# Optimization experiments

Hardware: AMD Instinct MI355X
Metric: run time of the kernel (lower is better)

The kernel has to match this reference:

```python
import jax, jax.numpy as jnp
import numpy as np

N_NODES = 100000   # m for both sparse matmuls (graph adjacency is N x N)
ITERATIONS = 10
ALPHA = 0.1
N_FEATURES = 2000
HIDDEN = 64
N_LABELS = 16
NNZ_FEAT = 5000000
N_EDGES = 3200000


def setup_inputs() -> dict:
    key = jax.random.key(0)
    ks = jax.random.split(key, 10)
    feat_rows = jax.random.randint(ks[0], (NNZ_FEAT,), 0, N_NODES, dtype=jnp.int32)
    feat_cols = jax.random.randint(ks[1], (NNZ_FEAT,), 0, N_FEATURES, dtype=jnp.int32)
    feature_values = jax.random.uniform(ks[2], (NNZ_FEAT,), dtype=jnp.float32)
    edge_rows = jax.random.randint(ks[3], (N_EDGES,), 0, N_NODES, dtype=jnp.int32)
    edge_cols = jax.random.randint(ks[4], (N_EDGES,), 0, N_NODES, dtype=jnp.int32)
    edge_weights = jax.random.uniform(ks[5], (N_EDGES,), dtype=jnp.float32) * (1.0 / 32.0)
    W1 = jax.random.normal(ks[6], (N_FEATURES, HIDDEN), dtype=jnp.float32) * 0.05
    b1 = jax.random.normal(ks[7], (HIDDEN,), dtype=jnp.float32) * 0.05
    W2 = jax.random.normal(ks[8], (HIDDEN, N_LABELS), dtype=jnp.float32) * 0.1
    b2 = jax.random.normal(ks[9], (N_LABELS,), dtype=jnp.float32) * 0.1
    return {"feat_rows": feat_rows, "feat_cols": feat_cols, "feature_values": feature_values,
            "edge_rows": edge_rows, "edge_cols": edge_cols, "edge_weights": edge_weights,
            "W1": W1, "b1": b1, "W2": W2, "b2": b2}


def spmm(rows, cols, vals, matrix, m):
    # sparse [m, k] (COO) @ dense [k, d]: gather rows of dense, scale, scatter-add
    out = matrix[cols] * vals[:, None]          # [nnz, d]
    return jax.ops.segment_sum(out, rows, num_segments=m)


def reference(feat_rows, feat_cols, feature_values, edge_rows, edge_cols,
              edge_weights, W1, b1, W2, b2):
    # layer 1: sparse features [N, F] @ W1 [F, H] + b1  (eval mode: dropout is identity)
    latent1 = spmm(feat_rows, feat_cols, feature_values, W1, N_NODES) + b1  # [N, H]
    latent1 = jax.nn.relu(latent1)
    z = latent1 @ W2 + b2                       # [N, L] local predictions

    def step(p, _):
        new = spmm(edge_rows, edge_cols, edge_weights, p, N_NODES)  # A_hat @ p
        p = (1.0 - ALPHA) * new + ALPHA * z
        return p, None

    preds, _ = jax.lax.scan(step, z, None, length=ITERATIONS)
    return jax.nn.log_softmax(preds, axis=1)
```

## Files before the change

kernel.cpp:

```cpp
#include <hip/hip_runtime.h>

#define N_NODES    100000
#define N_FEATURES 2000
#define HIDDEN     64
#define N_LABELS   16
#define NNZ_FEAT   5000000
#define N_EDGES    3200000
#define ITERS      10
#define ALPHA      0.1f

#define CBSH       9
#define CROWS      (1 << CBSH)
#define NBC        ((N_NODES + CROWS - 1) >> CBSH)
#define TILE       8192
#define NFB        ((NNZ_FEAT + TILE - 1) / TILE)
#define NEB        ((N_EDGES + TILE - 1) / TILE)
#define BCAP       28672

#define EQMUL  1048544.0f
#define EWDEC  (0.028125f / 32767.0f)

__device__ __forceinline__ unsigned short f2bf(float x) {
    unsigned u = __float_as_uint(x);
    u += 0x7FFF + ((u >> 16) & 1);
    return (unsigned short)(u >> 16);
}
__device__ __forceinline__ float bf_lo(unsigned u) { return __uint_as_float(u << 16); }
__device__ __forceinline__ float bf_hi(unsigned u) { return __uint_as_float(u & 0xFFFF0000u); }

__device__ __forceinline__ unsigned char f2fp8(float x) {
    float a = fabsf(x) * 16.0f;
    a = fminf(fmaxf(a, 0.015625f), 448.0f);
    unsigned u = __float_as_uint(a) + 0x80000;
    int v11 = (int)((u >> 20) & 0x7FF) - 960;
    v11 = v11 < 8 ? 8 : (v11 > 126 ? 126 : v11);
    return (unsigned char)(v11 | ((__float_as_uint(x) >> 24) & 0x80));
}
#if __has_builtin(__builtin_amdgcn_cvt_f32_fp8)
#define FP8DEC(w, s) __builtin_amdgcn_cvt_f32_fp8((w), (s))
#else
__device__ __forceinline__ float fp8dec_sw(unsigned w, int s) {
    unsigned u = (w >> (8 * s)) & 0xFF;
    return __uint_as_float((((u & 0x7F) + 960) << 20) | ((u & 0x80) << 24));
}
#define FP8DEC(w, s) fp8dec_sw((w), (s))
#endif


__global__ __launch_bounds__(256) void zero_int(int* __restrict__ p, int n) {
    int t = blockIdx.x * 256 + threadIdx.x;
    if (t < n) p[t] = 0;
}

__global__ __launch_bounds__(256) void hist2_k(const int* __restrict__ frows, int nf,
                                               int* __restrict__ cbf,
                                               const int* __restrict__ erows, int ne,
                                               int* __restrict__ cbe) {
    __shared__ int h[4 * NBC];
    for (int i = threadIdx.x; i < 4 * NBC; i += 256) h[i] = 0;
    __syncthreads();
    const int* rows; int n; int* dst; int b0, nb;
    if (blockIdx.x < 1280) { rows = frows; n = nf; dst = cbf; b0 = blockIdx.x; nb = 1280; }
    else                   { rows = erows; n = ne; dst = cbe; b0 = blockIdx.x - 1280; nb = 768; }
    int off = (threadIdx.x & 3) * NBC;
    int stride = nb * 256;
    for (int i = b0 * 256 + threadIdx.x; i < n; i += stride)
        atomicAdd(&h[off + (rows[i] >> CBSH)], 1);
    __syncthreads();
    for (int i = threadIdx.x; i < NBC; i += 256) {
        int v = h[i] + h[NBC + i] + h[2 * NBC + i] + h[3 * NBC + i];
        if (v) atomicAdd(&dst[i], v);
    }
}

__global__ __launch_bounds__(256) void scan2_k(const int* __restrict__ cbf,
                                               int* __restrict__ cbasef, int* __restrict__ gbf,
                                               int* __restrict__ frp,
                                               const int* __restrict__ cbe,
                                               int* __restrict__ cbasee, int* __restrict__ gbe,
                                               int* __restrict__ erp) {
    const int* cnt; int* cbase; int* gbcur; int* rp;
    if (blockIdx.x == 0) { cnt = cbf; cbase = cbasef; gbcur = gbf; rp = frp; }
    else                 { cnt = cbe; cbase = cbasee; gbcur = gbe; rp = erp; }
    __shared__ int s[256];
    int t = threadIdx.x;
    int v = (t < NBC) ? cnt[t] : 0;
    s[t] = v;
    __syncthreads();
    for (int off = 1; off < 256; off <<= 1) {
        int a = (t >= off) ? s[t - off] : 0;
        __syncthreads();
        s[t] += a;
        __syncthreads();
    }
    if (t < NBC) { cbase[t] = s[t] - v; gbcur[t] = s[t] - v; }
    if (t == NBC - 1) { cbase[NBC] = s[t]; rp[N_NODES] = s[t]; }
}

__global__ __launch_bounds__(1024) void binA2_k(
    const int* __restrict__ frows, const int* __restrict__ fcols, const float* __restrict__ fvals,
    int* __restrict__ gbf, int* __restrict__ fpk, unsigned short* __restrict__ frl,
    const int* __restrict__ erows, const int* __restrict__ ecols, const float* __restrict__ evals,
    int* __restrict__ gbe, int* __restrict__ epk, unsigned short* __restrict__ erl)
{
    __shared__ int            staged_pk[TILE];
    __shared__ unsigned short staged_rl[TILE];
    __shared__ unsigned char  sbkt[TILE];
    __shared__ int cnt0[NBC];
    __shared__ int cnt1[NBC];
    __shared__ int rstart[NBC];
    __shared__ int gbase[NBC];
    __shared__ int sc[256];

    const int* rows; const int* cols; const float* vals;
    int* gbcur; int* bpk; unsigned short* brl;
    int n, qshift, bfval; float qmul;
    int bid = blockIdx.x;
    if (bid < NFB) {
        rows = frows; cols = fcols; vals = fvals; gbcur = gbf; bpk = fpk; brl = frl;
        n = NNZ_FEAT; qshift = 16; qmul = 0.f; bfval = 1;
    } else {
        bid -= NFB;
        rows = erows; cols = ecols; vals = evals; gbcur = gbe; bpk = epk; brl = erl;
        n = N_EDGES; qshift = 17; qmul = EQMUL; bfval = 0;
    }

    int tid = threadIdx.x;
    int base = bid * TILE;
    int m = n - base; if (m > TILE) m = TILE;

    for (int i = tid; i < NBC; i += 1024) { cnt0[i] = 0; cnt1[i] = 0; }
    __syncthreads();

    int c = tid & 1;
    int* cntc = c ? cnt1 : cnt0;
    int seq[TILE / 1024];
    int rbuf[TILE / 1024];
    #pragma unroll
    for (int k = 0; k < TILE / 1024; ++k) {
        int j = k * 1024 + tid;
        if (j < m) {
            int r = rows[base + j];
            rbuf[k] = r;
            seq[k] = atomicAdd(&cntc[r >> CBSH], 1);
        }
    }
    __syncthreads();

    if (tid < 256) sc[tid] = (tid < NBC) ? (cnt0[tid] + cnt1[tid]) : 0;
    __syncthreads();
    for (int off = 1; off < 256; off <<= 1) {
        int a = 0;
        if (tid < 256 && tid >= off) a = sc[tid - off];
        __syncthreads();
        if (tid < 256) sc[tid] += a;
        __syncthreads();
    }
    if (tid < NBC) rstart[tid] = sc[tid] - (cnt0[tid] + cnt1[tid]);
    __syncthreads();

    #pragma unroll
    for (int k = 0; k < TILE / 1024; ++k) {
        int j = k * 1024 + tid;
        if (j < m) {
            int r = rbuf[k];
            int b = r >> CBSH;
            float v = vals[base + j];
            int q = bfval ? (int)f2bf(v) : __float2int_rn(v * qmul);
            int slot = rstart[b] + (c ? cnt0[b] : 0) + seq[k];
            staged_pk[slot] = (q << qshift) | cols[base + j];
            staged_rl[slot] = (unsigned short)(r & (CROWS - 1));
            sbkt[slot] = (unsigned char)b;
        }
    }
    __syncthreads();

    if (tid < NBC) {
        int tot = cnt0[tid] + cnt1[tid];
        if (tot > 0) gbase[tid] = atomicAdd(&gbcur[tid], tot);
    }
    __syncthreads();

    #pragma unroll
    for (int k = 0; k < TILE / 1024; ++k) {
        int slot = k * 1024 + tid;
        if (slot < m) {
            int b = sbkt[slot];
            int dst = gbase[b] + (slot - rstart[b]);
            bpk[dst] = staged_pk[slot];
            brl[dst] = staged_rl[slot];
        }
    }
}

__global__ __launch_bounds__(1024) void binB3_k(
    const int* __restrict__ fpk, const unsigned short* __restrict__ frl,
    const int* __restrict__ cbasef, int* __restrict__ frp, int* __restrict__ fcw,
    const int* __restrict__ epk, const unsigned short* __restrict__ erl,
    const int* __restrict__ cbasee, int* __restrict__ erp, int* __restrict__ ecw)
{
    const int* bin_pk; const unsigned short* bin_rl; const int* cbase; int* rp; int* cw;
    int b = blockIdx.x;
    if (b < NBC) { bin_pk = fpk; bin_rl = frl; cbase = cbasef; rp = frp; cw = fcw; }
    else { b -= NBC; bin_pk = epk; bin_rl = erl; cbase = cbasee; rp = erp; cw = ecw; }

    int r0 = b << CBSH;
    int nrows = N_NODES - r0; if (nrows > CROWS) nrows = CROWS;
    __shared__ int staged[BCAP];
    __shared__ int hist[CROWS];
    __shared__ int sc[CROWS];
    int t = threadIdx.x;
    if (t < CROWS) hist[t] = 0;
    __syncthreads();
    int s = cbase[b], e = cbase[b + 1];
    int cnt = e - s;
    for (int i = s + t; i < e; i += 1024)
        atomicAdd(&hist[bin_rl[i]], 1);
    __syncthreads();
    if (t < CROWS) sc[t] = hist[t];
    __syncthreads();
    for (int off = 1; off < CROWS; off <<= 1) {
        int a = (t >= off && t < CROWS) ? sc[t - off] : 0;
        __syncthreads();
        if (t < CROWS) sc[t] += a;
        __syncthreads();
    }
    if (t < CROWS) {
        int excl = sc[t] - hist[t];
        if (t < nrows) rp[r0 + t] = excl + s;
        hist[t] = excl;
    }
    __syncthreads();

    if (cnt <= BCAP) {
        for (int i = s + t; i < e; i += 1024) {
            int pos = atomicAdd(&hist[bin_rl[i]], 1);
            staged[pos] = bin_pk[i];
        }
        __syncthreads();
        for (int j = t; j < cnt; j += 1024)
            cw[s + j] = staged[j];
    } else {
        for (int i = s + t; i < e; i += 1024) {
            int pos = atomicAdd(&hist[bin_rl[i]], 1);
            cw[s + pos] = bin_pk[i];
        }
    }
}


__global__ __launch_bounds__(256) void w1_to_fp8(const float* __restrict__ W1,
                                                 unsigned char* __restrict__ W1q) {
    int t = blockIdx.x * 256 + threadIdx.x;
    if (t < N_FEATURES * HIDDEN / 4) {
        float4 v = reinterpret_cast<const float4*>(W1)[t];
        uchar4 o;
        o.x = f2fp8(v.x); o.y = f2fp8(v.y); o.z = f2fp8(v.z); o.w = f2fp8(v.w);
        reinterpret_cast<uchar4*>(W1q)[t] = o;
    }
}

__global__ __launch_bounds__(256) void spmm_fused(const int* __restrict__ rp,
                                                  const int* __restrict__ cwp,
                                                  const unsigned char* __restrict__ W1q,
                                                  const float* __restrict__ b1,
                                                  const float* __restrict__ W2,
                                                  const float* __restrict__ b2,
                                                  unsigned short* __restrict__ az,
                                                  unsigned short* __restrict__ pb0) {
    __shared__ float sW2T[N_LABELS * (HIDDEN + 1)];
    __shared__ float sb1[HIDDEN];
    __shared__ float sb2[N_LABELS];
    for (int i = threadIdx.x; i < HIDDEN * N_LABELS; i += 256) {
        int h = i >> 4, l = i & 15;
        sW2T[l * (HIDDEN + 1) + h] = W2[i];
    }
    if (threadIdx.x < HIDDEN) sb1[threadIdx.x] = b1[threadIdx.x];
    if (threadIdx.x < N_LABELS) sb2[threadIdx.x] = b2[threadIdx.x];
    __syncthreads();

    int t = blockIdx.x * 256 + threadIdx.x;
    int row = t >> 3, sl = t & 7;
    if (row >= N_NODES) return;
    int s = rp[row], e = rp[row + 1];
    int hbase = sl * 8;

    float acc[8];
    #pragma unroll
    for (int j = 0; j < 8; ++j) acc[j] = 0.f;

    int i = s;
    for (; i + 3 < e; i += 4) {
        uint2 wv[4]; float vv[4];
        #pragma unroll
        for (int k = 0; k < 4; ++k) {
            int pk = cwp[i + k];
            vv[k] = bf_hi((unsigned)pk);
            wv[k] = *reinterpret_cast<const uint2*>(W1q + (size_t)(pk & 0x7FF) * HIDDEN + hbase);
        }
        #pragma unroll
        for (int k = 0; k < 4; ++k) {
            acc[0] = fmaf(vv[k], FP8DEC(wv[k].x, 0), acc[0]);
            acc[1] = fmaf(vv[k], FP8DEC(wv[k].x, 1), acc[1]);
            acc[2] = fmaf(vv[k], FP8DEC(wv[k].x, 2), acc[2]);
            acc[3] = fmaf(vv[k], FP8DEC(wv[k].x, 3), acc[3]);
            acc[4] = fmaf(vv[k], FP8DEC(wv[k].y, 0), acc[4]);
            acc[5] = fmaf(vv[k], FP8DEC(wv[k].y, 1), acc[5]);
            acc[6] = fmaf(vv[k], FP8DEC(wv[k].y, 2), acc[6]);
            acc[7] = fmaf(vv[k], FP8DEC(wv[k].y, 3), acc[7]);
        }
    }
    for (; i < e; ++i) {
        int pk = cwp[i];
        float v = bf_hi((unsigned)pk);
        uint2 w = *reinterpret_cast<const uint2*>(W1q + (size_t)(pk & 0x7FF) * HIDDEN + hbase);
        acc[0] = fmaf(v, FP8DEC(w.x, 0), acc[0]);
        acc[1] = fmaf(v, FP8DEC(w.x, 1), acc[1]);
        acc[2] = fmaf(v, FP8DEC(w.x, 2), acc[2]);
        acc[3] = fmaf(v, FP8DEC(w.x, 3), acc[3]);
        acc[4] = fmaf(v, FP8DEC(w.y, 0), acc[4]);
        acc[5] = fmaf(v, FP8DEC(w.y, 1), acc[5]);
        acc[6] = fmaf(v, FP8DEC(w.y, 2), acc[6]);
        acc[7] = fmaf(v, FP8DEC(w.y, 3), acc[7]);
    }

    float part[16];
    #pragma unroll
    for (int l = 0; l < 16; ++l) part[l] = 0.f;
    #pragma unroll
    for (int j = 0; j < 8; ++j) {
        float a = fmaf(acc[j], 0.0625f, sb1[hbase + j]);
        a = a > 0.f ? a : 0.f;
        #pragma unroll
        for (int l = 0; l < 16; ++l)
            part[l] = fmaf(a, sW2T[l * (HIDDEN + 1) + hbase + j], part[l]);
    }
    #pragma unroll
    for (int l = 0; l < 8; ++l) {
        float lo = __shfl_xor(part[l], 1);
        float hi = __shfl_xor(part[l + 8], 1);
        part[l] = (sl & 1) ? (part[l + 8] + hi) : (part[l] + lo);
    }
    #pragma unroll
    for (int l = 0; l < 4; ++l) {
        float lo = __shfl_xor(part[l], 2);
        float hi = __shfl_xor(part[l + 4], 2);
        part[l] = (sl & 2) ? (part[l + 4] + hi) : (part[l] + lo);
    }
    #pragma unroll
    for (int l = 0; l < 2; ++l) {
        float lo = __shfl_xor(part[l], 4);
        float hi = __shfl_xor(part[l + 2], 4);
        part[l] = (sl & 4) ? (part[l + 2] + hi) : (part[l] + lo);
    }
    int lbase = 8 * (sl & 1) + 4 * ((sl >> 1) & 1) + 2 * ((sl >> 2) & 1);
    float z0 = part[0] + sb2[lbase];
    float z1 = part[1] + sb2[lbase + 1];
    unsigned oz = (unsigned)f2bf(z0) | ((unsigned)f2bf(z1) << 16);
    unsigned oa = (unsigned)f2bf(ALPHA * z0) | ((unsigned)f2bf(ALPHA * z1) << 16);
    *reinterpret_cast<unsigned*>(pb0 + (size_t)row * N_LABELS + lbase) = oz;
    *reinterpret_cast<unsigned*>(az  + (size_t)row * N_LABELS + lbase) = oa;
}

__global__ __launch_bounds__(256) void prop_bf16(const int* __restrict__ rp,
                                                 const int* __restrict__ cwp,
                                                 const unsigned short* __restrict__ az,
                                                 const unsigned short* __restrict__ pin,
                                                 unsigned short* __restrict__ pout) {
    int t = blockIdx.x * 256 + threadIdx.x;
    int row = t >> 3, sub = t & 7;
    if (row >= N_NODES) return;
    int s = rp[row], e = rp[row + 1];
    unsigned azw = *reinterpret_cast<const unsigned*>(az + (size_t)row * N_LABELS + sub * 2);
    float a0 = bf_lo(azw), a1 = bf_hi(azw);
    int i = s;
    for (; i + 7 < e; i += 8) {
        int cwv = cwp[i + sub];
        unsigned q[8]; float w[8];
        #pragma unroll
        for (int k = 0; k < 8; ++k) {
            int pk = __shfl(cwv, k, 8);
            w[k] = (float)((unsigned)pk >> 17) * EWDEC;
            q[k] = *reinterpret_cast<const unsigned*>(pin + (size_t)(pk & 0x1FFFF) * N_LABELS + sub * 2);
        }
        #pragma unroll
        for (int k = 0; k < 8; ++k) {
            a0 = fmaf(w[k], bf_lo(q[k]), a0);
            a1 = fmaf(w[k], bf_hi(q[k]), a1);
        }
    }
    for (; i < e; ++i) {
        int pk = cwp[i];
        float w = (float)((unsigned)pk >> 17) * EWDEC;
        unsigned q = *reinterpret_cast<const unsigned*>(pin + (size_t)(pk & 0x1FFFF) * N_LABELS + sub * 2);
        a0 = fmaf(w, bf_lo(q), a0);
        a1 = fmaf(w, bf_hi(q), a1);
    }
    *reinterpret_cast<unsigned*>(pout + (size_t)row * N_LABELS + sub * 2) =
        (unsigned)f2bf(a0) | ((unsigned)f2bf(a1) << 16);
}

__global__ __launch_bounds__(256) void prop_final(const int* __restrict__ rp,
                                                  const int* __restrict__ cwp,
                                                  const unsigned short* __restrict__ az,
                                                  const unsigned short* __restrict__ pin,
                                                  float* __restrict__ out) {
    int t = blockIdx.x * 256 + threadIdx.x;
    int row = t >> 3, sub = t & 7;
    if (row >= N_NODES) return;
    int s = rp[row], e = rp[row + 1];
    unsigned azw = *reinterpret_cast<const unsigned*>(az + (size_t)row * N_LABELS + sub * 2);
    float a0 = bf_lo(azw), a1 = bf_hi(azw);
    int i = s;
    for (; i + 7 < e; i += 8) {
        int cwv = cwp[i + sub];
        unsigned q[8]; float w[8];
        #pragma unroll
        for (int k = 0; k < 8; ++k) {
            int pk = __shfl(cwv, k, 8);
            w[k] = (float)((unsigned)pk >> 17) * EWDEC;
            q[k] = *reinterpret_cast<const unsigned*>(pin + (size_t)(pk & 0x1FFFF) * N_LABELS + sub * 2);
        }
        #pragma unroll
        for (int k = 0; k < 8; ++k) {
            a0 = fmaf(w[k], bf_lo(q[k]), a0);
            a1 = fmaf(w[k], bf_hi(q[k]), a1);
        }
    }
    for (; i < e; ++i) {
        int pk = cwp[i];
        float w = (float)((unsigned)pk >> 17) * EWDEC;
        unsigned q = *reinterpret_cast<const unsigned*>(pin + (size_t)(pk & 0x1FFFF) * N_LABELS + sub * 2);
        a0 = fmaf(w, bf_lo(q), a0);
        a1 = fmaf(w, bf_hi(q), a1);
    }
    float m = fmaxf(a0, a1);
    m = fmaxf(m, __shfl_xor(m, 1));
    m = fmaxf(m, __shfl_xor(m, 2));
    m = fmaxf(m, __shfl_xor(m, 4));
    float ssum = __expf(a0 - m) + __expf(a1 - m);
    ssum += __shfl_xor(ssum, 1);
    ssum += __shfl_xor(ssum, 2);
    ssum += __shfl_xor(ssum, 4);
    float lse = m + __logf(ssum);
    *reinterpret_cast<float2*>(out + (size_t)row * N_LABELS + sub * 2) =
        make_float2(a0 - lse, a1 - lse);
}


__global__ __launch_bounds__(256) void zero_f4(float4* __restrict__ p, int n4) {
    int t = blockIdx.x * 256 + threadIdx.x;
    if (t < n4) p[t] = make_float4(0.f, 0.f, 0.f, 0.f);
}

__global__ __launch_bounds__(256) void spmm_feat_atomic(
    const int* __restrict__ rows, const int* __restrict__ cols,
    const float* __restrict__ vals, const float* __restrict__ W1,
    float* __restrict__ latent)
{
    long long t = (long long)blockIdx.x * 256 + threadIdx.x;
    if (t >= (long long)NNZ_FEAT * 16) return;
    int e  = (int)(t >> 4);
    int dg = (int)(t & 15);
    int r = rows[e]; int c = cols[e]; float v = vals[e];
    float4 w = *reinterpret_cast<const float4*>(W1 + (size_t)c * HIDDEN + dg * 4);
    float* dst = latent + (size_t)r * HIDDEN + dg * 4;
    atomicAdd(dst + 0, v * w.x); atomicAdd(dst + 1, v * w.y);
    atomicAdd(dst + 2, v * w.z); atomicAdd(dst + 3, v * w.w);
}

__global__ __launch_bounds__(256) void compute_z(const float* __restrict__ latent,
                                                 const float* __restrict__ b1,
                                                 const float* __restrict__ W2,
                                                 const float* __restrict__ b2,
                                                 float* __restrict__ z) {
    __shared__ float sW2[HIDDEN * N_LABELS];
    __shared__ float sb1[HIDDEN];
    for (int i = threadIdx.x; i < HIDDEN * N_LABELS; i += 256) sW2[i] = W2[i];
    if (threadIdx.x < HIDDEN) sb1[threadIdx.x] = b1[threadIdx.x];
    __syncthreads();
    int t = blockIdx.x * 256 + threadIdx.x;
    int node = t >> 4;
    int l = t & 15;
    if (node >= N_NODES) return;
    float acc = b2[l];
    const float* lat = latent + (size_t)node * HIDDEN;
    #pragma unroll 8
    for (int h = 0; h < HIDDEN; ++h) {
        float a = lat[h] + sb1[h];
        a = a > 0.f ? a : 0.f;
        acc = fmaf(a, sW2[h * N_LABELS + l], acc);
    }
    z[(size_t)node * N_LABELS + l] = acc;
}

__global__ __launch_bounds__(256) void init_acc(const float* __restrict__ z,
                                                float* __restrict__ acc) {
    int t = blockIdx.x * 256 + threadIdx.x;
    if (t < N_NODES * N_LABELS / 4) {
        float4 zv = reinterpret_cast<const float4*>(z)[t];
        reinterpret_cast<float4*>(acc)[t] =
            make_float4(ALPHA * zv.x, ALPHA * zv.y, ALPHA * zv.z, ALPHA * zv.w);
    }
}

__global__ __launch_bounds__(256) void edge_scatter(
    const int* __restrict__ rows, const int* __restrict__ cols,
    const float* __restrict__ w, const float* __restrict__ p,
    float* __restrict__ acc)
{
    long long t = (long long)blockIdx.x * 256 + threadIdx.x;
    if (t >= (long long)N_EDGES * 4) return;
    int e = (int)(t >> 2);
    int part = (int)(t & 3);
    int r = rows[e]; int c = cols[e];
    float wt = w[e] * (1.0f - ALPHA);
    float4 pv = *reinterpret_cast<const float4*>(p + (size_t)c * N_LABELS + part * 4);
    float* dst = acc + (size_t)r * N_LABELS + part * 4;
    atomicAdd(dst + 0, wt * pv.x); atomicAdd(dst + 1, wt * pv.y);
    atomicAdd(dst + 2, wt * pv.z); atomicAdd(dst + 3, wt * pv.w);
}

__global__ __launch_bounds__(256) void logsoftmax_k(const float* __restrict__ p,
                                                    float* __restrict__ out) {
    int node = blockIdx.x * 256 + threadIdx.x;
    if (node >= N_NODES) return;
    const float4* src = reinterpret_cast<const float4*>(p + (size_t)node * N_LABELS);
    float4 a = src[0], b = src[1], c = src[2], d = src[3];
    float x[16] = {a.x,a.y,a.z,a.w, b.x,b.y,b.z,b.w, c.x,c.y,c.z,c.w, d.x,d.y,d.z,d.w};
    float m = x[0];
    #pragma unroll
    for (int i = 1; i < 16; ++i) m = fmaxf(m, x[i]);
    float s = 0.f;
    #pragma unroll
    for (int i = 0; i < 16; ++i) s += expf(x[i] - m);
    float lse = m + logf(s);
    float4* o = reinterpret_cast<float4*>(out + (size_t)node * N_LABELS);
    o[0] = make_float4(x[0]-lse,  x[1]-lse,  x[2]-lse,  x[3]-lse);
    o[1] = make_float4(x[4]-lse,  x[5]-lse,  x[6]-lse,  x[7]-lse);
    o[2] = make_float4(x[8]-lse,  x[9]-lse,  x[10]-lse, x[11]-lse);
    o[3] = make_float4(x[12]-lse, x[13]-lse, x[14]-lse, x[15]-lse);
}


extern "C" void kernel_launch(void* const* d_in, const int* in_sizes, int n_in,
                              void* d_out, int out_size, void* d_ws, size_t ws_size,
                              hipStream_t stream)
{
    const int*   feat_rows = (const int*)d_in[0];
    const int*   feat_cols = (const int*)d_in[1];
    const float* feat_vals = (const float*)d_in[2];
    const int*   edge_rows = (const int*)d_in[3];
    const int*   edge_cols = (const int*)d_in[4];
    const float* edge_w    = (const float*)d_in[5];
    const float* W1 = (const float*)d_in[6];
    const float* b1 = (const float*)d_in[7];
    const float* W2 = (const float*)d_in[8];
    const float* b2 = (const float*)d_in[9];
    float* out = (float*)d_out;

    size_t need = 0;
    size_t o_feat_cw = need; need += (size_t)NNZ_FEAT;
    size_t o_edge_cw = need; need += (size_t)N_EDGES;
    size_t o_latent  = need; need += (size_t)N_NODES * HIDDEN;
    size_t o_z       = need; need += (size_t)N_NODES * N_LABELS;
    size_t o_p0      = need; need += (size_t)N_NODES * N_LABELS;
    size_t o_p1      = need; need += (size_t)N_NODES * N_LABELS;
    size_t o_frp     = need; need += N_NODES + 1;
    size_t o_erp     = need; need += N_NODES + 1;
    size_t o_w1q     = need; need += (size_t)N_FEATURES * HIDDEN / 4;
    size_t o_ebin_pk = need; need += (size_t)N_EDGES;
    size_t o_ebin_rl = need; need += (size_t)N_EDGES / 2;
    size_t o_cbf     = need; need += NBC;
    size_t o_cbe     = need; need += NBC;
    size_t o_cbasef  = need; need += NBC + 1;
    size_t o_cbasee  = need; need += NBC + 1;
    size_t o_gbf     = need; need += NBC;
    size_t o_gbe     = need; need += NBC;
    size_t need_bytes = need * 4 + 64;

    float* base = (float*)d_ws;
    float* latent = base + o_latent;
    float* z  = base + o_z;
    float* p0 = base + o_p0;
    float* p1 = base + o_p1;

    if (ws_size >= need_bytes) {
        int* feat_cw = (int*)(base + o_feat_cw);
        int* edge_cw = (int*)(base + o_edge_cw);
        int* feat_rp = (int*)(base + o_frp);
        int* edge_rp = (int*)(base + o_erp);
        unsigned char* W1q = (unsigned char*)(base + o_w1q);
        int* cbf    = (int*)(base + o_cbf);
        int* cbe    = (int*)(base + o_cbe);
        int* cbasef = (int*)(base + o_cbasef);
        int* cbasee = (int*)(base + o_cbasee);
        int* gbf    = (int*)(base + o_gbf);
        int* gbe    = (int*)(base + o_gbe);
        int*            fbin_pk = (int*)(base + o_latent);
        unsigned short* fbin_rl = (unsigned short*)(base + o_z);
        int*            ebin_pk = (int*)(base + o_ebin_pk);
        unsigned short* ebin_rl = (unsigned short*)(base + o_ebin_rl);
        unsigned short* az  = (unsigned short*)z;
        unsigned short* pb0 = (unsigned short*)p0;
        unsigned short* pb1 = (unsigned short*)p1;

        w1_to_fp8<<<(N_FEATURES * HIDDEN / 4 + 255) / 256, 256, 0, stream>>>(W1, W1q);
        zero_int<<<2, 256, 0, stream>>>(cbf, 2 * NBC);
        hist2_k<<<2048, 256, 0, stream>>>(feat_rows, NNZ_FEAT, cbf, edge_rows, N_EDGES, cbe);
        scan2_k<<<2, 256, 0, stream>>>(cbf, cbasef, gbf, feat_rp, cbe, cbasee, gbe, edge_rp);
        binA2_k<<<NFB + NEB, 1024, 0, stream>>>(
            feat_rows, feat_cols, feat_vals, gbf, fbin_pk, fbin_rl,
            edge_rows, edge_cols, edge_w, gbe, ebin_pk, ebin_rl);
        binB3_k<<<2 * NBC, 1024, 0, stream>>>(
            fbin_pk, fbin_rl, cbasef, feat_rp, feat_cw,
            ebin_pk, ebin_rl, cbasee, edge_rp, edge_cw);

        spmm_fused<<<(N_NODES * 8 + 255) / 256, 256, 0, stream>>>(
            feat_rp, feat_cw, W1q, b1, W2, b2, az, pb0);

        const unsigned short* pin = pb0;
        int pgrid = (N_NODES * 8 + 255) / 256;
        for (int it = 0; it < ITERS - 1; ++it) {
            unsigned short* pout = (it & 1) ? pb0 : pb1;
            prop_bf16<<<pgrid, 256, 0, stream>>>(edge_rp, edge_cw, az, pin, pout);
            pin = pout;
        }
        prop_final<<<pgrid, 256, 0, stream>>>(edge_rp, edge_cw, az, pin, out);
    } else {
        int n4 = N_NODES * HIDDEN / 4;
        zero_f4<<<(n4 + 255) / 256, 256, 0, stream>>>((float4*)latent, n4);
        long long total = (long long)NNZ_FEAT * 16;
        spmm_feat_atomic<<<(int)((total + 255) / 256), 256, 0, stream>>>(
            feat_rows, feat_cols, feat_vals, W1, latent);
        compute_z<<<N_NODES * 16 / 256, 256, 0, stream>>>(latent, b1, W2, b2, z);
        const float* pin = z;
        float* bufs[2] = {p0, p1};
        for (int it = 0; it < ITERS; ++it) {
            float* pout = bufs[it & 1];
            init_acc<<<(N_NODES * N_LABELS / 4 + 255) / 256, 256, 0, stream>>>(z, pout);
            long long tot = (long long)N_EDGES * 4;
            edge_scatter<<<(int)((tot + 255) / 256), 256, 0, stream>>>(
                edge_rows, edge_cols, edge_w, pin, pout);
            pin = pout;
        }
        logsoftmax_k<<<(N_NODES + 255) / 256, 256, 0, stream>>>(pin, out);
    }
}
```

Before: 461.4 us.

## Vectorize COO loads in histogram/binning and stage fp8 W1 in shared memory

The histogram kernel now reads row indices as int4 and does four shared atomics per load. The binning kernel gives each thread 8 contiguous entries read with vector loads, and it drops the two-way split counters in favour of a single counter array. The fused feature SpMM stages the whole fp8 W1 (padded stride 9) into LDS and runs 1024-thread blocks, so the W1 gather hits shared memory instead of global. Risks: roughly 144KB of LDS per block limits occupancy to one block per CU and adds a staging cost per block, and the int4 histogram loop silently drops any tail when n is not a multiple of 4.

```diff
diff --git a/kernel.cpp b/kernel.cpp
--- a/kernel.cpp
+++ b/kernel.cpp
@@ -64,8 +64,15 @@
     else                   { rows = erows; n = ne; dst = cbe; b0 = blockIdx.x - 1280; nb = 768; }
     int off = (threadIdx.x & 3) * NBC;
     int stride = nb * 256;
-    for (int i = b0 * 256 + threadIdx.x; i < n; i += stride)
-        atomicAdd(&h[off + (rows[i] >> CBSH)], 1);
+    int n4 = n >> 2;
+    const int4* rows4 = reinterpret_cast<const int4*>(rows);
+    for (int i = b0 * 256 + threadIdx.x; i < n4; i += stride) {
+        int4 r = rows4[i];
+        atomicAdd(&h[off + (r.x >> CBSH)], 1);
+        atomicAdd(&h[off + (r.y >> CBSH)], 1);
+        atomicAdd(&h[off + (r.z >> CBSH)], 1);
+        atomicAdd(&h[off + (r.w >> CBSH)], 1);
+    }
     __syncthreads();
     for (int i = threadIdx.x; i < NBC; i += 256) {
         int v = h[i] + h[NBC + i] + h[2 * NBC + i] + h[3 * NBC + i];
@@ -106,8 +113,7 @@
     __shared__ int            staged_pk[TILE];
     __shared__ unsigned short staged_rl[TILE];
     __shared__ unsigned char  sbkt[TILE];
-    __shared__ int cnt0[NBC];
-    __shared__ int cnt1[NBC];
+    __shared__ int cnt[NBC];
     __shared__ int rstart[NBC];
     __shared__ int gbase[NBC];
     __shared__ int sc[256];
@@ -129,25 +135,39 @@
     int base = bid * TILE;
     int m = n - base; if (m > TILE) m = TILE;
 
-    for (int i = tid; i < NBC; i += 1024) { cnt0[i] = 0; cnt1[i] = 0; }
-    __syncthreads();
-
-    int c = tid & 1;
-    int* cntc = c ? cnt1 : cnt0;
-    int seq[TILE / 1024];
-    int rbuf[TILE / 1024];
-    #pragma unroll
-    for (int k = 0; k < TILE / 1024; ++k) {
-        int j = k * 1024 + tid;
-        if (j < m) {
-            int r = rows[base + j];
-            rbuf[k] = r;
-            seq[k] = atomicAdd(&cntc[r >> CBSH], 1);
-        }
-    }
-    __syncthreads();
-
-    if (tid < 256) sc[tid] = (tid < NBC) ? (cnt0[tid] + cnt1[tid]) : 0;
+    for (int i = tid; i < NBC; i += 1024) cnt[i] = 0;
+    __syncthreads();
+
+    int rbuf[8]; int cbuf[8]; float vbuf[8]; int seq[8];
+    int j0 = tid * 8;
+    if (m == TILE) {
+        const int4* r4 = reinterpret_cast<const int4*>(rows + base) + tid * 2;
+        const int4* c4 = reinterpret_cast<const int4*>(cols + base) + tid * 2;
+        const float4* v4 = reinterpret_cast<const float4*>(vals + base) + tid * 2;
+        int4 ra = r4[0], rb = r4[1];
+        int4 ca = c4[0], cb = c4[1];
+        float4 va = v4[0], vb = v4[1];
+        rbuf[0]=ra.x; rbuf[1]=ra.y; rbuf[2]=ra.z; rbuf[3]=ra.w;
+        rbuf[4]=rb.x; rbuf[5]=rb.y; rbuf[6]=rb.z; rbuf[7]=rb.w;
+        cbuf[0]=ca.x; cbuf[1]=ca.y; cbuf[2]=ca.z; cbuf[3]=ca.w;
+        cbuf[4]=cb.x; cbuf[5]=cb.y; cbuf[6]=cb.z; cbuf[7]=cb.w;
+        vbuf[0]=va.x; vbuf[1]=va.y; vbuf[2]=va.z; vbuf[3]=va.w;
+        vbuf[4]=vb.x; vbuf[5]=vb.y; vbuf[6]=vb.z; vbuf[7]=vb.w;
+    } else {
+        #pragma unroll
+        for (int k = 0; k < 8; ++k) {
+            int j = j0 + k;
+            if (j < m) { rbuf[k] = rows[base + j]; cbuf[k] = cols[base + j]; vbuf[k] = vals[base + j]; }
+        }
+    }
+    #pragma unroll
+    for (int k = 0; k < 8; ++k) {
+        int j = j0 + k;
+        if (j < m) seq[k] = atomicAdd(&cnt[rbuf[k] >> CBSH], 1);
+    }
+    __syncthreads();
+
+    if (tid < 256) sc[tid] = (tid < NBC) ? cnt[tid] : 0;
     __syncthreads();
     for (int off = 1; off < 256; off <<= 1) {
         int a = 0;
@@ -156,33 +176,29 @@
         if (tid < 256) sc[tid] += a;
         __syncthreads();
     }
-    if (tid < NBC) rstart[tid] = sc[tid] - (cnt0[tid] + cnt1[tid]);
-    __syncthreads();
-
-    #pragma unroll
-    for (int k = 0; k < TILE / 1024; ++k) {
-        int j = k * 1024 + tid;
+    if (tid < NBC) rstart[tid] = sc[tid] - cnt[tid];
+    __syncthreads();
+
+    #pragma unroll
+    for (int k = 0; k < 8; ++k) {
+        int j = j0 + k;
         if (j < m) {
             int r = rbuf[k];
             int b = r >> CBSH;
-            float v = vals[base + j];
-            int q = bfval ? (int)f2bf(v) : __float2int_rn(v * qmul);
-            int slot = rstart[b] + (c ? cnt0[b] : 0) + seq[k];
-            staged_pk[slot] = (q << qshift) | cols[base + j];
+            int q = bfval ? (int)f2bf(vbuf[k]) : __float2int_rn(vbuf[k] * qmul);
+            int slot = rstart[b] + seq[k];
+            staged_pk[slot] = (q << qshift) | cbuf[k];
             staged_rl[slot] = (unsigned short)(r & (CROWS - 1));
             sbkt[slot] = (unsigned char)b;
         }
     }
     __syncthreads();
 
-    if (tid < NBC) {
-        int tot = cnt0[tid] + cnt1[tid];
-        if (tot > 0) gbase[tid] = atomicAdd(&gbcur[tid], tot);
-    }
-    __syncthreads();
-
-    #pragma unroll
-    for (int k = 0; k < TILE / 1024; ++k) {
+    if (tid < NBC && cnt[tid] > 0) gbase[tid] = atomicAdd(&gbcur[tid], cnt[tid]);
+    __syncthreads();
+
+    #pragma unroll
+    for (int k = 0; k < 8; ++k) {
         int slot = k * 1024 + tid;
         if (slot < m) {
             int b = sbkt[slot];
@@ -260,18 +276,22 @@
     }
 }
 
-__global__ __launch_bounds__(256) void spmm_fused(const int* __restrict__ rp,
-                                                  const int* __restrict__ cwp,
-                                                  const unsigned char* __restrict__ W1q,
-                                                  const float* __restrict__ b1,
-                                                  const float* __restrict__ W2,
-                                                  const float* __restrict__ b2,
-                                                  unsigned short* __restrict__ az,
-                                                  unsigned short* __restrict__ pb0) {
+__global__ __launch_bounds__(1024) void spmm_fused(const int* __restrict__ rp,
+                                                   const int* __restrict__ cwp,
+                                                   const unsigned char* __restrict__ W1q,
+                                                   const float* __restrict__ b1,
+                                                   const float* __restrict__ W2,
+                                                   const float* __restrict__ b2,
+                                                   unsigned short* __restrict__ az,
+                                                   unsigned short* __restrict__ pb0) {
+    __shared__ uint2 sW1[N_FEATURES * 9];
     __shared__ float sW2T[N_LABELS * (HIDDEN + 1)];
     __shared__ float sb1[HIDDEN];
     __shared__ float sb2[N_LABELS];
-    for (int i = threadIdx.x; i < HIDDEN * N_LABELS; i += 256) {
+    const uint2* w18 = reinterpret_cast<const uint2*>(W1q);
+    for (int i = threadIdx.x; i < N_FEATURES * 8; i += 1024)
+        sW1[(i >> 3) * 9 + (i & 7)] = w18[i];
+    for (int i = threadIdx.x; i < HIDDEN * N_LABELS; i += 1024) {
         int h = i >> 4, l = i & 15;
         sW2T[l * (HIDDEN + 1) + h] = W2[i];
     }
@@ -279,11 +299,10 @@
     if (threadIdx.x < N_LABELS) sb2[threadIdx.x] = b2[threadIdx.x];
     __syncthreads();
 
-    int t = blockIdx.x * 256 + threadIdx.x;
+    int t = blockIdx.x * 1024 + threadIdx.x;
     int row = t >> 3, sl = t & 7;
     if (row >= N_NODES) return;
     int s = rp[row], e = rp[row + 1];
-    int hbase = sl * 8;
 
     float acc[8];
     #pragma unroll
@@ -296,7 +315,7 @@
         for (int k = 0; k < 4; ++k) {
             int pk = cwp[i + k];
             vv[k] = bf_hi((unsigned)pk);
-            wv[k] = *reinterpret_cast<const uint2*>(W1q + (size_t)(pk & 0x7FF) * HIDDEN + hbase);
+            wv[k] = sW1[(pk & 0x7FF) * 9 + sl];
         }
         #pragma unroll
         for (int k = 0; k < 4; ++k) {
@@ -313,7 +332,7 @@
     for (; i < e; ++i) {
         int pk = cwp[i];
         float v = bf_hi((unsigned)pk);
-        uint2 w = *reinterpret_cast<const uint2*>(W1q + (size_t)(pk & 0x7FF) * HIDDEN + hbase);
+        uint2 w = sW1[(pk & 0x7FF) * 9 + sl];
         acc[0] = fmaf(v, FP8DEC(w.x, 0), acc[0]);
         acc[1] = fmaf(v, FP8DEC(w.x, 1), acc[1]);
         acc[2] = fmaf(v, FP8DEC(w.x, 2), acc[2]);
@@ -329,6 +348,7 @@
     for (int l = 0; l < 16; ++l) part[l] = 0.f;
     #pragma unroll
     for (int j = 0; j < 8; ++j) {
+        int hbase = sl * 8;
         float a = fmaf(acc[j], 0.0625f, sb1[hbase + j]);
         a = a > 0.f ? a : 0.f;
         #pragma unroll
@@ -616,7 +636,7 @@
             fbin_pk, fbin_rl, cbasef, feat_rp, feat_cw,
             ebin_pk, ebin_rl, cbasee, edge_rp, edge_cw);
 
-        spmm_fused<<<(N_NODES * 8 + 255) / 256, 256, 0, stream>>>(
+        spmm_fused<<<(N_NODES * 8 + 1023) / 1024, 1024, 0, stream>>>(
             feat_rp, feat_cw, W1q, b1, W2, b2, az, pb0);
 
         const unsigned short* pin = pb0;
```

Result: no change. 465.2 us (+0.8%).
